# Kernel tuning notes

Measured on AMD Instinct MI355X. Metric: run time of the kernel, lower is better.

Reference implementation:

```python
import jax, jax.numpy as jnp
import numpy as np

D_MODEL = 512
SRC_LEN = 256
TGT_LEN = 256
EPS = 1e-8


def setup_inputs() -> dict:
    key = jax.random.key(0)
    k1, k2, k3, k4, k5, k6 = jax.random.split(key, 6)
    B = 8
    dec = jax.random.normal(k1, (B, TGT_LEN, D_MODEL), dtype=jnp.float32)
    enc = jax.random.normal(k2, (B, SRC_LEN, D_MODEL), dtype=jnp.float32)
    input_lengths = jax.random.randint(k3, (B,), 1, SRC_LEN + 1)
    # torch Linear(d_model, src_length) weights, stored transposed for x @ W
    s = 1.0 / np.sqrt(D_MODEL)
    W1 = jax.random.uniform(k4, (D_MODEL, SRC_LEN), minval=-s, maxval=s, dtype=jnp.float32)
    W2 = jax.random.uniform(k5, (D_MODEL, SRC_LEN), minval=-s, maxval=s, dtype=jnp.float32)
    sv = 1.0 / np.sqrt(SRC_LEN)
    vt = jax.random.uniform(k6, (SRC_LEN,), minval=-sv, maxval=sv, dtype=jnp.float32)
    return {"decoder_hidden_states": dec, "encoder_hidden_states": enc,
            "input_lengths": input_lengths, "W1": W1, "W2": W2, "vt": vt}


def reference(decoder_hidden_states, encoder_hidden_states, input_lengths, W1, W2, vt):
    B, src, _ = encoder_hidden_states.shape
    dt = jnp.einsum('btd,dl->btl', decoder_hidden_states, W1)   # [B,tgt,L]
    et = jnp.einsum('bsd,dl->bsl', encoder_hidden_states, W2)   # [B,src,L]
    # [B,tgt,src,L] broadcast add + tanh, reduced by vt -> [B,tgt,src]
    scores = jnp.einsum('btsl,l->bts', jnp.tanh(dt[:, :, None, :] + et[:, None, :, :]), vt)
    mask = (jnp.arange(src) < input_lengths[:, None])[:, None, :]  # [B,1,src]
    scores = scores + jnp.log(mask.astype(scores.dtype) + EPS)
    log_score = jax.nn.log_softmax(scores, axis=-1)             # over src
    return jnp.swapaxes(log_score, -1, -2)                      # [B,src,tgt]
```

## Files before the change

### kernel.cpp

```cpp
#include <hip/hip_runtime.h>
#include <hip/hip_bf16.h>

#define TGT 256
#define SRC 256
#define LDIM 256
#define DM 512
#define BATCH 8

#define C2LOG2E 2.8853902f
#define LOG2E 1.4426950f
#define LN2 0.6931472f
#define LOGEPS -18.420681f

#if __has_builtin(__builtin_amdgcn_exp2f)
#define EXP2F(x) __builtin_amdgcn_exp2f(x)
#else
#define EXP2F(x) exp2f(x)
#endif
#if __has_builtin(__builtin_amdgcn_rcpf)
#define RCPF(x) __builtin_amdgcn_rcpf(x)
#else
#define RCPF(x) (1.0f / (x))
#endif
#if __has_builtin(__builtin_amdgcn_logf)
#define LOG2F_(x) __builtin_amdgcn_logf(x)
#else
#define LOG2F_(x) __log2f(x)
#endif

typedef short bf16x8 __attribute__((ext_vector_type(8)));
typedef float f32x4 __attribute__((ext_vector_type(4)));

__device__ __forceinline__ unsigned int f2b_pk(float lo, float hi) {
    union { float f; unsigned int u; } a, b;
    a.f = lo; b.f = hi;
    unsigned int ra = (a.u + 0x7fffu + ((a.u >> 16) & 1u)) >> 16;
    unsigned int rb = (b.u + 0x7fffu + ((b.u >> 16) & 1u)) >> 16;
    return (ra & 0xffffu) | (rb << 16);
}

__global__ __launch_bounds__(256) void wtrans_k(
    const float* __restrict__ W1, const float* __restrict__ W2,
    unsigned short* __restrict__ Wt)
{
    __shared__ float tile[32][33];
    const int mat = blockIdx.z;
    const float* __restrict__ W = mat ? W2 : W1;
    unsigned short* __restrict__ dst = Wt + (size_t)mat * LDIM * DM;
    const int k0 = blockIdx.x * 32, n0 = blockIdx.y * 32;
    const int tx = threadIdx.x & 31, ty = threadIdx.x >> 5;
    #pragma unroll
    for (int i = 0; i < 32; i += 8)
        tile[ty + i][tx] = W[(size_t)(k0 + ty + i) * LDIM + n0 + tx];
    __syncthreads();
    #pragma unroll
    for (int i = 0; i < 32; i += 8) {
        union { float f; unsigned int u; } v; v.f = tile[tx][ty + i];
        dst[(size_t)(n0 + ty + i) * DM + k0 + tx] =
            (unsigned short)((v.u + 0x7fffu + ((v.u >> 16) & 1u)) >> 16);
    }
}

#define APITCH 72

__global__ __launch_bounds__(256) void gemm_k(
    const float* __restrict__ dec, const float* __restrict__ enc,
    const unsigned short* __restrict__ Wt, float* __restrict__ E)
{
    __shared__ unsigned short As[64 * APITCH];
    __shared__ unsigned short Bs[64 * APITCH];

    const int tid = threadIdx.x;
    const int m0 = blockIdx.y * 64;
    const int n0 = blockIdx.x * 64;
    const bool is_dec = (m0 < 2048);
    const float* __restrict__ X = is_dec ? dec : enc;
    const unsigned short* __restrict__ Wm = Wt + (is_dec ? 0 : (size_t)LDIM * DM);
    const int xr0 = is_dec ? m0 : m0 - 2048;

    const int arow = tid >> 2;
    const int aseg = (tid & 3) << 4;
    const float* __restrict__ aptr = X + (size_t)(xr0 + arow) * DM + aseg;
    const unsigned short* __restrict__ bptr = Wm + (size_t)(n0 + arow) * DM + aseg;

    const int wave = tid >> 6;
    const int lane = tid & 63;
    const int l15 = lane & 15;
    const int quad = lane >> 4;

    f32x4 acc[4] = {};
    float4 a0, a1, a2, a3;
    uint4 bb0, bb1;

    a0 = *(const float4*)(aptr + 0);
    a1 = *(const float4*)(aptr + 4);
    a2 = *(const float4*)(aptr + 8);
    a3 = *(const float4*)(aptr + 12);
    bb0 = *(const uint4*)(bptr + 0);
    bb1 = *(const uint4*)(bptr + 8);

    for (int it = 0; it < DM / 64; ++it) {
        if (it) __syncthreads();
        uint4 wa0, wa1;
        wa0.x = f2b_pk(a0.x, a0.y); wa0.y = f2b_pk(a0.z, a0.w);
        wa0.z = f2b_pk(a1.x, a1.y); wa0.w = f2b_pk(a1.z, a1.w);
        wa1.x = f2b_pk(a2.x, a2.y); wa1.y = f2b_pk(a2.z, a2.w);
        wa1.z = f2b_pk(a3.x, a3.y); wa1.w = f2b_pk(a3.z, a3.w);
        *(uint4*)&As[arow * APITCH + aseg]     = wa0;
        *(uint4*)&As[arow * APITCH + aseg + 8] = wa1;
        *(uint4*)&Bs[arow * APITCH + aseg]     = bb0;
        *(uint4*)&Bs[arow * APITCH + aseg + 8] = bb1;
        __syncthreads();
        if (it < DM / 64 - 1) {
            const int ko = (it + 1) * 64;
            a0 = *(const float4*)(aptr + ko + 0);
            a1 = *(const float4*)(aptr + ko + 4);
            a2 = *(const float4*)(aptr + ko + 8);
            a3 = *(const float4*)(aptr + ko + 12);
            bb0 = *(const uint4*)(bptr + ko + 0);
            bb1 = *(const uint4*)(bptr + ko + 8);
        }
        #pragma unroll
        for (int kb = 0; kb < 64; kb += 32) {
            const bf16x8 af = *(const bf16x8*)&As[(wave * 16 + l15) * APITCH + kb + quad * 8];
            #pragma unroll
            for (int c = 0; c < 4; ++c) {
                const bf16x8 bf = *(const bf16x8*)&Bs[(c * 16 + l15) * APITCH + kb + quad * 8];
                acc[c] = __builtin_amdgcn_mfma_f32_16x16x32_bf16(af, bf, acc[c], 0, 0, 0);
            }
        }
    }

    const int orow = m0 + wave * 16 + quad * 4;
    const int ocol = n0 + l15;
    #pragma unroll
    for (int c = 0; c < 4; ++c)
        #pragma unroll
        for (int r = 0; r < 4; ++r)
            E[(size_t)(orow + r) * LDIM + ocol + c * 16] = EXP2F(acc[c][r] * C2LOG2E);
}

__global__ __launch_bounds__(256) void scores_k(
    const float* __restrict__ E, const int* __restrict__ lens,
    const float* __restrict__ vt, float* __restrict__ out)
{
    __shared__ __align__(16) float dtr[LDIM][4];
    __shared__ __align__(16) float vt2s[LDIM];
    __shared__ float4 wred[4];

    const int s = threadIdx.x;
    const int b = blockIdx.y;
    const int t0 = blockIdx.x * 4;
    const float* __restrict__ Ed = E;
    const float* __restrict__ Ee = E + (size_t)2048 * LDIM;

    #pragma unroll
    for (int i = 0; i < 4; ++i)
        dtr[s][i] = Ed[(size_t)(b * TGT + t0 + i) * LDIM + s];
    vt2s[s] = -2.0f * vt[s];
    __syncthreads();

    const int len_b = lens[b];
    float4 acc = {0.f, 0.f, 0.f, 0.f};
    const float4* __restrict__ erow = (const float4*)(Ee + (size_t)(b * SRC + s) * LDIM);

    for (int l0 = 0; l0 < LDIM; l0 += 4) {
        const float4 e4 = erow[l0 >> 2];
        const float4 v4 = *(const float4*)&vt2s[l0];
        const float ee[4] = {e4.x, e4.y, e4.z, e4.w};
        const float vv[4] = {v4.x, v4.y, v4.z, v4.w};
        #pragma unroll
        for (int j = 0; j < 4; ++j) {
            const float4 d4 = *(const float4*)&dtr[l0 + j][0];
            acc.x = fmaf(vv[j], RCPF(1.0f + d4.x * ee[j]), acc.x);
            acc.y = fmaf(vv[j], RCPF(1.0f + d4.y * ee[j]), acc.y);
            acc.z = fmaf(vv[j], RCPF(1.0f + d4.z * ee[j]), acc.z);
            acc.w = fmaf(vv[j], RCPF(1.0f + d4.w * ee[j]), acc.w);
        }
    }

    const float madd = (s < len_b) ? 0.0f : LOGEPS;
    acc.x += madd; acc.y += madd; acc.z += madd; acc.w += madd;

    const int wid = s >> 6, lane = s & 63;

    float4 r = acc;
    #pragma unroll
    for (int off = 32; off > 0; off >>= 1) {
        r.x = fmaxf(r.x, __shfl_down(r.x, off));
        r.y = fmaxf(r.y, __shfl_down(r.y, off));
        r.z = fmaxf(r.z, __shfl_down(r.z, off));
        r.w = fmaxf(r.w, __shfl_down(r.w, off));
    }
    if (lane == 0) wred[wid] = r;
    __syncthreads();
    float4 mx = wred[0];
    #pragma unroll
    for (int w = 1; w < 4; ++w) {
        mx.x = fmaxf(mx.x, wred[w].x);
        mx.y = fmaxf(mx.y, wred[w].y);
        mx.z = fmaxf(mx.z, wred[w].z);
        mx.w = fmaxf(mx.w, wred[w].w);
    }
    __syncthreads();

    float4 ex;
    ex.x = EXP2F((acc.x - mx.x) * LOG2E);
    ex.y = EXP2F((acc.y - mx.y) * LOG2E);
    ex.z = EXP2F((acc.z - mx.z) * LOG2E);
    ex.w = EXP2F((acc.w - mx.w) * LOG2E);
    float4 sr = ex;
    #pragma unroll
    for (int off = 32; off > 0; off >>= 1) {
        sr.x += __shfl_down(sr.x, off);
        sr.y += __shfl_down(sr.y, off);
        sr.z += __shfl_down(sr.z, off);
        sr.w += __shfl_down(sr.w, off);
    }
    if (lane == 0) wred[wid] = sr;
    __syncthreads();
    float4 sm = wred[0];
    #pragma unroll
    for (int w = 1; w < 4; ++w) {
        sm.x += wred[w].x; sm.y += wred[w].y; sm.z += wred[w].z; sm.w += wred[w].w;
    }

    float4 o;
    o.x = acc.x - (mx.x + LOG2F_(sm.x) * LN2);
    o.y = acc.y - (mx.y + LOG2F_(sm.y) * LN2);
    o.z = acc.z - (mx.z + LOG2F_(sm.z) * LN2);
    o.w = acc.w - (mx.w + LOG2F_(sm.w) * LN2);
    *(float4*)(out + (size_t)(b * SRC + s) * TGT + t0) = o;
}

extern "C" void kernel_launch(void* const* d_in, const int* in_sizes, int n_in,
                              void* d_out, int out_size, void* d_ws, size_t ws_size,
                              hipStream_t stream) {
    const float* dec = (const float*)d_in[0];
    const float* enc = (const float*)d_in[1];
    const int* lens  = (const int*)d_in[2];
    const float* W1  = (const float*)d_in[3];
    const float* W2  = (const float*)d_in[4];
    const float* vt  = (const float*)d_in[5];
    float* out = (float*)d_out;

    unsigned short* Wt = (unsigned short*)d_ws;
    float* E = (float*)((char*)d_ws + (size_t)2 * LDIM * DM * sizeof(unsigned short));

    wtrans_k<<<dim3(16, 8, 2), 256, 0, stream>>>(W1, W2, Wt);
    gemm_k<<<dim3(LDIM / 64, 4096 / 64), 256, 0, stream>>>(dec, enc, Wt, E);
    scores_k<<<dim3(TGT / 4, BATCH), 256, 0, stream>>>(E, lens, vt, out);
}
```

Measured before the change: 98.40 us.

## Pair reciprocals in scores, split L across half-blocks, widen GEMM to 512 threads

The scores kernel now combines two tanh terms over one shared denominator, so it needs one reciprocal per pair of L elements instead of one per element. Each block uses 512 threads: the two halves each reduce half of the L dimension, and their partial sums are merged through shared memory before the softmax. The GEMM also moves to 512 threads in a 4x2 wave layout with smaller per-thread loads. The aim is to cut transcendental-unit pressure and raise occupancy, at the cost of extra multiplies, some overflow risk in the product of denominators, and idle half-blocks during the softmax.

```diff
diff --git a/kernel.cpp b/kernel.cpp
--- a/kernel.cpp
+++ b/kernel.cpp
@@ -63,7 +63,7 @@
 
 #define APITCH 72
 
-__global__ __launch_bounds__(256) void gemm_k(
+__global__ __launch_bounds__(512) void gemm_k(
     const float* __restrict__ dec, const float* __restrict__ enc,
     const unsigned short* __restrict__ Wt, float* __restrict__ E)
 {
@@ -78,159 +78,184 @@
     const unsigned short* __restrict__ Wm = Wt + (is_dec ? 0 : (size_t)LDIM * DM);
     const int xr0 = is_dec ? m0 : m0 - 2048;
 
-    const int arow = tid >> 2;
-    const int aseg = (tid & 3) << 4;
-    const float* __restrict__ aptr = X + (size_t)(xr0 + arow) * DM + aseg;
-    const unsigned short* __restrict__ bptr = Wm + (size_t)(n0 + arow) * DM + aseg;
+    const int arow = tid >> 3;
+    const int aoff = (tid & 7) << 3;
+    const float* __restrict__ aptr = X + (size_t)(xr0 + arow) * DM + aoff;
+    const unsigned short* __restrict__ bptr = Wm + (size_t)(n0 + arow) * DM + aoff;
 
     const int wave = tid >> 6;
     const int lane = tid & 63;
     const int l15 = lane & 15;
     const int quad = lane >> 4;
-
-    f32x4 acc[4] = {};
-    float4 a0, a1, a2, a3;
-    uint4 bb0, bb1;
+    const int wm = wave >> 1;
+    const int wn = wave & 1;
+
+    f32x4 acc[2] = {};
+    float4 a0, a1;
+    uint4 bb;
 
     a0 = *(const float4*)(aptr + 0);
     a1 = *(const float4*)(aptr + 4);
-    a2 = *(const float4*)(aptr + 8);
-    a3 = *(const float4*)(aptr + 12);
-    bb0 = *(const uint4*)(bptr + 0);
-    bb1 = *(const uint4*)(bptr + 8);
+    bb = *(const uint4*)(bptr);
 
     for (int it = 0; it < DM / 64; ++it) {
         if (it) __syncthreads();
-        uint4 wa0, wa1;
-        wa0.x = f2b_pk(a0.x, a0.y); wa0.y = f2b_pk(a0.z, a0.w);
-        wa0.z = f2b_pk(a1.x, a1.y); wa0.w = f2b_pk(a1.z, a1.w);
-        wa1.x = f2b_pk(a2.x, a2.y); wa1.y = f2b_pk(a2.z, a2.w);
-        wa1.z = f2b_pk(a3.x, a3.y); wa1.w = f2b_pk(a3.z, a3.w);
-        *(uint4*)&As[arow * APITCH + aseg]     = wa0;
-        *(uint4*)&As[arow * APITCH + aseg + 8] = wa1;
-        *(uint4*)&Bs[arow * APITCH + aseg]     = bb0;
-        *(uint4*)&Bs[arow * APITCH + aseg + 8] = bb1;
+        uint4 wa;
+        wa.x = f2b_pk(a0.x, a0.y); wa.y = f2b_pk(a0.z, a0.w);
+        wa.z = f2b_pk(a1.x, a1.y); wa.w = f2b_pk(a1.z, a1.w);
+        *(uint4*)&As[arow * APITCH + aoff] = wa;
+        *(uint4*)&Bs[arow * APITCH + aoff] = bb;
         __syncthreads();
         if (it < DM / 64 - 1) {
             const int ko = (it + 1) * 64;
             a0 = *(const float4*)(aptr + ko + 0);
             a1 = *(const float4*)(aptr + ko + 4);
-            a2 = *(const float4*)(aptr + ko + 8);
-            a3 = *(const float4*)(aptr + ko + 12);
-            bb0 = *(const uint4*)(bptr + ko + 0);
-            bb1 = *(const uint4*)(bptr + ko + 8);
+            bb = *(const uint4*)(bptr + ko);
         }
         #pragma unroll
         for (int kb = 0; kb < 64; kb += 32) {
-            const bf16x8 af = *(const bf16x8*)&As[(wave * 16 + l15) * APITCH + kb + quad * 8];
+            const bf16x8 af = *(const bf16x8*)&As[(wm * 16 + l15) * APITCH + kb + quad * 8];
             #pragma unroll
-            for (int c = 0; c < 4; ++c) {
-                const bf16x8 bf = *(const bf16x8*)&Bs[(c * 16 + l15) * APITCH + kb + quad * 8];
+            for (int c = 0; c < 2; ++c) {
+                const bf16x8 bf = *(const bf16x8*)&Bs[(wn * 32 + c * 16 + l15) * APITCH + kb + quad * 8];
                 acc[c] = __builtin_amdgcn_mfma_f32_16x16x32_bf16(af, bf, acc[c], 0, 0, 0);
             }
         }
     }
 
-    const int orow = m0 + wave * 16 + quad * 4;
-    const int ocol = n0 + l15;
-    #pragma unroll
-    for (int c = 0; c < 4; ++c)
+    const int orow = m0 + wm * 16 + quad * 4;
+    const int ocol = n0 + wn * 32 + l15;
+    #pragma unroll
+    for (int c = 0; c < 2; ++c)
         #pragma unroll
         for (int r = 0; r < 4; ++r)
             E[(size_t)(orow + r) * LDIM + ocol + c * 16] = EXP2F(acc[c][r] * C2LOG2E);
 }
 
-__global__ __launch_bounds__(256) void scores_k(
+__device__ __forceinline__ void pair_acc(
+    const float4 d0, const float4 d1, const float e0, const float e1,
+    const float v0, const float v1, float4& acc)
+{
+    float4 p0, p1, num, den;
+    p0.x = fmaf(d0.x, e0, 1.f); p0.y = fmaf(d0.y, e0, 1.f);
+    p0.z = fmaf(d0.z, e0, 1.f); p0.w = fmaf(d0.w, e0, 1.f);
+    p1.x = fmaf(d1.x, e1, 1.f); p1.y = fmaf(d1.y, e1, 1.f);
+    p1.z = fmaf(d1.z, e1, 1.f); p1.w = fmaf(d1.w, e1, 1.f);
+    num.x = fmaf(v1, p0.x, v0 * p1.x); num.y = fmaf(v1, p0.y, v0 * p1.y);
+    num.z = fmaf(v1, p0.z, v0 * p1.z); num.w = fmaf(v1, p0.w, v0 * p1.w);
+    den.x = p0.x * p1.x; den.y = p0.y * p1.y;
+    den.z = p0.z * p1.z; den.w = p0.w * p1.w;
+    acc.x = fmaf(num.x, RCPF(den.x), acc.x);
+    acc.y = fmaf(num.y, RCPF(den.y), acc.y);
+    acc.z = fmaf(num.z, RCPF(den.z), acc.z);
+    acc.w = fmaf(num.w, RCPF(den.w), acc.w);
+}
+
+__global__ __launch_bounds__(512) void scores_k(
     const float* __restrict__ E, const int* __restrict__ lens,
     const float* __restrict__ vt, float* __restrict__ out)
 {
     __shared__ __align__(16) float dtr[LDIM][4];
     __shared__ __align__(16) float vt2s[LDIM];
+    __shared__ __align__(16) float4 accs[256];
     __shared__ float4 wred[4];
 
-    const int s = threadIdx.x;
+    const int tid = threadIdx.x;
+    const int s = tid & 255;
+    const int h = tid >> 8;
     const int b = blockIdx.y;
     const int t0 = blockIdx.x * 4;
     const float* __restrict__ Ed = E;
     const float* __restrict__ Ee = E + (size_t)2048 * LDIM;
 
     #pragma unroll
-    for (int i = 0; i < 4; ++i)
+    for (int i = h; i < 4; i += 2)
         dtr[s][i] = Ed[(size_t)(b * TGT + t0 + i) * LDIM + s];
-    vt2s[s] = -2.0f * vt[s];
-    __syncthreads();
-
-    const int len_b = lens[b];
+    if (tid < 256) vt2s[tid] = -2.0f * vt[tid];
+    __syncthreads();
+
     float4 acc = {0.f, 0.f, 0.f, 0.f};
-    const float4* __restrict__ erow = (const float4*)(Ee + (size_t)(b * SRC + s) * LDIM);
-
-    for (int l0 = 0; l0 < LDIM; l0 += 4) {
-        const float4 e4 = erow[l0 >> 2];
+    const float* __restrict__ erow = Ee + (size_t)(b * SRC + s) * LDIM;
+
+    const int lbase = h * 128;
+    for (int l0 = lbase; l0 < lbase + 128; l0 += 4) {
+        const float4 e4 = *(const float4*)(erow + l0);
         const float4 v4 = *(const float4*)&vt2s[l0];
-        const float ee[4] = {e4.x, e4.y, e4.z, e4.w};
-        const float vv[4] = {v4.x, v4.y, v4.z, v4.w};
-        #pragma unroll
-        for (int j = 0; j < 4; ++j) {
-            const float4 d4 = *(const float4*)&dtr[l0 + j][0];
-            acc.x = fmaf(vv[j], RCPF(1.0f + d4.x * ee[j]), acc.x);
-            acc.y = fmaf(vv[j], RCPF(1.0f + d4.y * ee[j]), acc.y);
-            acc.z = fmaf(vv[j], RCPF(1.0f + d4.z * ee[j]), acc.z);
-            acc.w = fmaf(vv[j], RCPF(1.0f + d4.w * ee[j]), acc.w);
-        }
-    }
-
-    const float madd = (s < len_b) ? 0.0f : LOGEPS;
-    acc.x += madd; acc.y += madd; acc.z += madd; acc.w += madd;
-
-    const int wid = s >> 6, lane = s & 63;
-
-    float4 r = acc;
-    #pragma unroll
-    for (int off = 32; off > 0; off >>= 1) {
-        r.x = fmaxf(r.x, __shfl_down(r.x, off));
-        r.y = fmaxf(r.y, __shfl_down(r.y, off));
-        r.z = fmaxf(r.z, __shfl_down(r.z, off));
-        r.w = fmaxf(r.w, __shfl_down(r.w, off));
-    }
-    if (lane == 0) wred[wid] = r;
-    __syncthreads();
-    float4 mx = wred[0];
-    #pragma unroll
-    for (int w = 1; w < 4; ++w) {
-        mx.x = fmaxf(mx.x, wred[w].x);
-        mx.y = fmaxf(mx.y, wred[w].y);
-        mx.z = fmaxf(mx.z, wred[w].z);
-        mx.w = fmaxf(mx.w, wred[w].w);
-    }
-    __syncthreads();
-
-    float4 ex;
-    ex.x = EXP2F((acc.x - mx.x) * LOG2E);
-    ex.y = EXP2F((acc.y - mx.y) * LOG2E);
-    ex.z = EXP2F((acc.z - mx.z) * LOG2E);
-    ex.w = EXP2F((acc.w - mx.w) * LOG2E);
-    float4 sr = ex;
-    #pragma unroll
-    for (int off = 32; off > 0; off >>= 1) {
-        sr.x += __shfl_down(sr.x, off);
-        sr.y += __shfl_down(sr.y, off);
-        sr.z += __shfl_down(sr.z, off);
-        sr.w += __shfl_down(sr.w, off);
-    }
-    if (lane == 0) wred[wid] = sr;
-    __syncthreads();
-    float4 sm = wred[0];
-    #pragma unroll
-    for (int w = 1; w < 4; ++w) {
-        sm.x += wred[w].x; sm.y += wred[w].y; sm.z += wred[w].z; sm.w += wred[w].w;
-    }
-
-    float4 o;
-    o.x = acc.x - (mx.x + LOG2F_(sm.x) * LN2);
-    o.y = acc.y - (mx.y + LOG2F_(sm.y) * LN2);
-    o.z = acc.z - (mx.z + LOG2F_(sm.z) * LN2);
-    o.w = acc.w - (mx.w + LOG2F_(sm.w) * LN2);
-    *(float4*)(out + (size_t)(b * SRC + s) * TGT + t0) = o;
+        const float4 d0 = *(const float4*)&dtr[l0 + 0][0];
+        const float4 d1 = *(const float4*)&dtr[l0 + 1][0];
+        const float4 d2 = *(const float4*)&dtr[l0 + 2][0];
+        const float4 d3 = *(const float4*)&dtr[l0 + 3][0];
+        pair_acc(d0, d1, e4.x, e4.y, v4.x, v4.y, acc);
+        pair_acc(d2, d3, e4.z, e4.w, v4.z, v4.w, acc);
+    }
+
+    if (h == 1) accs[s] = acc;
+    __syncthreads();
+
+    const int wid = tid >> 6, lane = tid & 63;
+    float4 mx, sm;
+
+    if (h == 0) {
+        const float4 o4 = accs[s];
+        acc.x += o4.x; acc.y += o4.y; acc.z += o4.z; acc.w += o4.w;
+        const float madd = (s < lens[b]) ? 0.0f : LOGEPS;
+        acc.x += madd; acc.y += madd; acc.z += madd; acc.w += madd;
+
+        float4 r = acc;
+        #pragma unroll
+        for (int off = 32; off > 0; off >>= 1) {
+            r.x = fmaxf(r.x, __shfl_down(r.x, off));
+            r.y = fmaxf(r.y, __shfl_down(r.y, off));
+            r.z = fmaxf(r.z, __shfl_down(r.z, off));
+            r.w = fmaxf(r.w, __shfl_down(r.w, off));
+        }
+        if (lane == 0) wred[wid] = r;
+    }
+    __syncthreads();
+
+    if (h == 0) {
+        mx = wred[0];
+        #pragma unroll
+        for (int w = 1; w < 4; ++w) {
+            mx.x = fmaxf(mx.x, wred[w].x);
+            mx.y = fmaxf(mx.y, wred[w].y);
+            mx.z = fmaxf(mx.z, wred[w].z);
+            mx.w = fmaxf(mx.w, wred[w].w);
+        }
+    }
+    __syncthreads();
+
+    if (h == 0) {
+        float4 ex;
+        ex.x = EXP2F((acc.x - mx.x) * LOG2E);
+        ex.y = EXP2F((acc.y - mx.y) * LOG2E);
+        ex.z = EXP2F((acc.z - mx.z) * LOG2E);
+        ex.w = EXP2F((acc.w - mx.w) * LOG2E);
+        float4 sr = ex;
+        #pragma unroll
+        for (int off = 32; off > 0; off >>= 1) {
+            sr.x += __shfl_down(sr.x, off);
+            sr.y += __shfl_down(sr.y, off);
+            sr.z += __shfl_down(sr.z, off);
+            sr.w += __shfl_down(sr.w, off);
+        }
+        if (lane == 0) wred[wid] = sr;
+    }
+    __syncthreads();
+
+    if (h == 0) {
+        sm = wred[0];
+        #pragma unroll
+        for (int w = 1; w < 4; ++w) {
+            sm.x += wred[w].x; sm.y += wred[w].y; sm.z += wred[w].z; sm.w += wred[w].w;
+        }
+        float4 o;
+        o.x = acc.x - (mx.x + LOG2F_(sm.x) * LN2);
+        o.y = acc.y - (mx.y + LOG2F_(sm.y) * LN2);
+        o.z = acc.z - (mx.z + LOG2F_(sm.z) * LN2);
+        o.w = acc.w - (mx.w + LOG2F_(sm.w) * LN2);
+        *(float4*)(out + (size_t)(b * SRC + s) * TGT + t0) = o;
+    }
 }
 
 extern "C" void kernel_launch(void* const* d_in, const int* in_sizes, int n_in,
@@ -248,6 +273,6 @@
     float* E = (float*)((char*)d_ws + (size_t)2 * LDIM * DM * sizeof(unsigned short));
 
     wtrans_k<<<dim3(16, 8, 2), 256, 0, stream>>>(W1, W2, Wt);
-    gemm_k<<<dim3(LDIM / 64, 4096 / 64), 256, 0, stream>>>(dec, enc, Wt, E);
-    scores_k<<<dim3(TGT / 4, BATCH), 256, 0, stream>>>(E, lens, vt, out);
-}
+    gemm_k<<<dim3(LDIM / 64, 4096 / 64), 512, 0, stream>>>(dec, enc, Wt, E);
+    scores_k<<<dim3(TGT / 4, BATCH), 512, 0, stream>>>(E, lens, vt, out);
+}
```

Result: no change. 98.12 us (-0.3%).
